# Optimization experiments

Hardware: AMD Instinct MI355X
Metric: run time of the kernel (lower is better)

## Reference

```python
import jax, jax.numpy as jnp
import numpy as np

HEAD_SIZE = 64
EMBED_DIM = 1024
SEQ_LEN = 4096
BATCH = 4


def setup_inputs() -> dict:
    key = jax.random.key(0)
    kx, kk, kq, kv = jax.random.split(key, 4)
    x = jax.random.normal(kx, (BATCH, SEQ_LEN, EMBED_DIM), dtype=jnp.float32)
    # nn.Linear(embedding_dim, head_size, bias=False): weight [head_size, embed];
    # store transposed [embed, head_size] so projection is x @ W.
    scale = 1.0 / np.sqrt(EMBED_DIM)
    Wk = jax.random.uniform(kk, (EMBED_DIM, HEAD_SIZE), jnp.float32, -scale, scale)
    Wq = jax.random.uniform(kq, (EMBED_DIM, HEAD_SIZE), jnp.float32, -scale, scale)
    Wv = jax.random.uniform(kv, (EMBED_DIM, HEAD_SIZE), jnp.float32, -scale, scale)
    return {"x": x, "Wk": Wk, "Wq": Wq, "Wv": Wv}


def reference(x, Wk, Wq, Wv):
    B, T, C = x.shape
    k = x @ Wk  # [B, T, H]
    q = x @ Wq  # [B, T, H]
    v = x @ Wv  # [B, T, H]
    H = k.shape[-1]
    s = jnp.einsum('bth,bsh->bts', q, k) * (H ** -0.5)  # [B, T, T]
    causal = jnp.tril(jnp.ones((T, T), dtype=bool))
    s = jnp.where(causal, s, -jnp.inf)
    a = jax.nn.softmax(s, axis=-1)  # dropout p=0.0 -> identity
    z = jnp.einsum('bts,bsh->bth', a, v)  # [B, T, H]
    return z
```

## Files before the change

### kernel.cpp

```cpp
#include <hip/hip_runtime.h>

#define SEQ 4096
#define EMB 1024
#define HS 64

typedef __attribute__((ext_vector_type(8))) short bf16x8;
typedef __attribute__((ext_vector_type(4))) float f32x4;

__device__ __forceinline__ unsigned short f2b(float f) {
    union { float f; unsigned u; } v; v.f = f;
    unsigned r = v.u + 0x7fffu + ((v.u >> 16) & 1u);
    return (unsigned short)(r >> 16);
}
__device__ __forceinline__ float b2f(unsigned short h) {
    union { unsigned u; float f; } v; v.u = ((unsigned)h) << 16;
    return v.f;
}
template <typename T>
__device__ __forceinline__ void gll16(const T* g, void* l) {
    __builtin_amdgcn_global_load_lds(
        (const __attribute__((address_space(1))) unsigned int*)(g),
        (__attribute__((address_space(3))) unsigned int*)(l), 16, 0, 0);
}

__global__ __launch_bounds__(256) void wt_kernel(const float* __restrict__ Wq,
                                                 const float* __restrict__ Wk,
                                                 const float* __restrict__ Wv,
                                                 unsigned short* __restrict__ Wt) {
    int id = blockIdx.x * 256 + threadIdx.x;
    int mat = id >> 16;
    int rem = id & 65535;
    int k = rem >> 6;
    int n = rem & 63;
    const float* W = (mat == 0) ? Wq : (mat == 1) ? Wk : Wv;
    float scale = (mat == 0) ? 0.125f * 1.44269504f : 1.0f;
    Wt[(mat * HS + n) * EMB + k] = f2b(W[k * HS + n] * scale);
}

__global__ __launch_bounds__(256, 2) void proj_kernel(const float* __restrict__ x,
                                                      const unsigned short* __restrict__ Wt,
                                                      unsigned short* __restrict__ Qb,
                                                      unsigned short* __restrict__ Kb,
                                                      unsigned short* __restrict__ Vt) {
    __shared__ float xf[2][32 * 64];
    __shared__ unsigned short wb[2][192 * 64];
    const int tid = threadIdx.x;
    const int wave = tid >> 6, lane = tid & 63;
    const int col = lane & 15, quad = lane >> 4;
    const int m0 = blockIdx.x * 32;
    const int b = m0 >> 12, t0 = m0 & 4095;

    const int xr_in = lane >> 4;
    const int xc = lane & 15;
    const int wr_in = lane >> 3;
    const int wc = lane & 7;

    f32x4 acc[2][3];
    #pragma unroll
    for (int i = 0; i < 2; i++)
        #pragma unroll
        for (int j = 0; j < 3; j++) acc[i][j] = (f32x4){0.f, 0.f, 0.f, 0.f};

    auto stage = [&](int k0, int bufi) {
        #pragma unroll
        for (int t = 0; t < 2; t++) {
            int R = (wave + t * 4) * 4;
            int row = R + xr_in;
            gll16(x + (size_t)(m0 + row) * EMB + k0 + ((xc ^ (row & 15)) << 2),
                  &xf[bufi][R * 64]);
        }
        #pragma unroll
        for (int t = 0; t < 6; t++) {
            int R = (wave * 6 + t) * 8;
            int row = R + wr_in;
            gll16(Wt + (size_t)row * EMB + k0 + ((wc ^ (row & 7)) << 3),
                  &wb[bufi][R * 64]);
        }
    };

    stage(0, 0);
    int buf = 0;
    #pragma unroll 1
    for (int k0 = 0; k0 < EMB; k0 += 64) {
        __syncthreads();
        if (k0 + 64 < EMB) stage(k0 + 64, buf ^ 1);
        #pragma unroll
        for (int kc = 0; kc < 2; kc++) {
            const int q2 = quad + kc * 4;
            bf16x8 af[2], bfr[3];
            #pragma unroll
            for (int mt = 0; mt < 2; mt++) {
                int rr = mt * 16 + col;
                float4 lo = *(const float4*)&xf[buf][rr * 64 + (((2 * q2) ^ col) << 2)];
                float4 hi = *(const float4*)&xf[buf][rr * 64 + (((2 * q2 + 1) ^ col) << 2)];
                bf16x8 a;
                a[0] = (short)f2b(lo.x); a[1] = (short)f2b(lo.y);
                a[2] = (short)f2b(lo.z); a[3] = (short)f2b(lo.w);
                a[4] = (short)f2b(hi.x); a[5] = (short)f2b(hi.y);
                a[6] = (short)f2b(hi.z); a[7] = (short)f2b(hi.w);
                af[mt] = a;
            }
            #pragma unroll
            for (int nt = 0; nt < 3; nt++) {
                int rn = wave * 48 + nt * 16 + col;
                bfr[nt] = *(const bf16x8*)&wb[buf][rn * 64 + ((q2 ^ (col & 7)) << 3)];
            }
            #pragma unroll
            for (int mt = 0; mt < 2; mt++)
                #pragma unroll
                for (int nt = 0; nt < 3; nt++)
                    acc[mt][nt] = __builtin_amdgcn_mfma_f32_16x16x32_bf16(af[mt], bfr[nt], acc[mt][nt], 0, 0, 0);
        }
        buf ^= 1;
    }

    #pragma unroll
    for (int mt = 0; mt < 2; mt++)
        #pragma unroll
        for (int nt = 0; nt < 3; nt++) {
            const int g = wave * 3 + nt;
            const int mat = g >> 2;
            const int ncol = (g & 3) * 16 + col;
            #pragma unroll
            for (int r = 0; r < 4; r++) {
                unsigned short val = f2b(acc[mt][nt][r]);
                int row = mt * 16 + quad * 4 + r;
                if (mat == 0)      Qb[(size_t)(m0 + row) * HS + ncol] = val;
                else if (mat == 1) Kb[(size_t)(m0 + row) * HS + ncol] = val;
                else               Vt[((size_t)b * HS + ncol) * SEQ + t0 + row] = val;
            }
        }
}

__global__ __launch_bounds__(256, 3) void attn_kernel(const unsigned short* __restrict__ Qb,
                                                      const unsigned short* __restrict__ Kb,
                                                      const unsigned short* __restrict__ Vt,
                                                      unsigned short* __restrict__ Opart,
                                                      float* __restrict__ Lpart) {
    __shared__ unsigned short Kl[2][64 * 64];
    __shared__ unsigned short Vl[2][64 * 64];
    __shared__ unsigned short P_lds[4][16 * 72];
    const int tid = threadIdx.x;
    const int wave = tid >> 6, lane = tid & 63;
    const int col = lane & 15, quad = lane >> 4;
    const int bid = blockIdx.x;
    const int g = 287 - (bid >> 2);
    const int b = bid & 3;
    int T = 0, accp = 0;
    for (;;) { int np = (T + 8) >> 3; if (accp + np > g) break; accp += np; T++; }
    const int piece = g - accp;
    const int q0 = T << 6;
    const int s_beg = piece << 3;
    const int s_end = min(s_beg + 8, T + 1);

    const unsigned short* Kp = Kb + ((size_t)(b << 12)) * HS;
    const unsigned short* Vp = Vt + (size_t)b * HS * SEQ;

    bf16x8 qf[2];
    #pragma unroll
    for (int c = 0; c < 2; c++)
        qf[c] = *(const bf16x8*)(Qb + ((size_t)(b << 12) + q0 + wave * 16 + col) * HS + quad * 8 + c * 32);

    f32x4 o[4];
    float l[4];
    #pragma unroll
    for (int ct = 0; ct < 4; ct++) o[ct] = (f32x4){0.f, 0.f, 0.f, 0.f};
    #pragma unroll
    for (int r = 0; r < 4; r++) l[r] = 0.f;

    const int r_in = lane >> 3;
    const int ch = lane & 7;

    auto stage = [&](int s, int bufi) {
        const int kv0 = s << 6;
        #pragma unroll
        for (int t = 0; t < 2; t++) {
            int R = (wave + t * 4) * 8;
            int row = R + r_in;
            gll16(Kp + (size_t)(kv0 + row) * HS + ((ch ^ (row & 7)) << 3), &Kl[bufi][R * 64]);
            gll16(Vp + (size_t)row * SEQ + kv0 + ((ch ^ (row & 7)) << 3), &Vl[bufi][R * 64]);
        }
    };

    stage(s_beg, 0);
    int buf = 0;
    const int rgb = q0 + wave * 16 + quad * 4;
    unsigned short* Pl = P_lds[wave];

    #pragma unroll 1
    for (int s = s_beg; s < s_end; s++) {
        __syncthreads();
        if (s + 1 < s_end) stage(s + 1, buf ^ 1);
        const int kv0 = s << 6;

        f32x4 sacc[4];
        #pragma unroll
        for (int ct = 0; ct < 4; ct++) sacc[ct] = (f32x4){0.f, 0.f, 0.f, 0.f};
        #pragma unroll
        for (int ct = 0; ct < 4; ct++) {
            int n = ct * 16 + col;
            #pragma unroll
            for (int kc = 0; kc < 2; kc++) {
                bf16x8 kf = *(const bf16x8*)&Kl[buf][n * 64 + (((kc * 4 + quad) ^ (col & 7)) << 3)];
                sacc[ct] = __builtin_amdgcn_mfma_f32_16x16x32_bf16(qf[kc], kf, sacc[ct], 0, 0, 0);
            }
        }

        float p[4][4];
        #pragma unroll
        for (int ct = 0; ct < 4; ct++) {
            int cg = kv0 + ct * 16 + col;
            #pragma unroll
            for (int r = 0; r < 4; r++) {
                float e = __builtin_exp2f(sacc[ct][r]);
                e = (cg > rgb + r) ? 0.f : e;
                p[ct][r] = e;
                l[r] += e;
            }
        }

        #pragma unroll
        for (int ct = 0; ct < 4; ct++)
            #pragma unroll
            for (int r = 0; r < 4; r++)
                Pl[(quad * 4 + r) * 72 + ct * 16 + col] = f2b(p[ct][r]);
        bf16x8 pf[2];
        #pragma unroll
        for (int c = 0; c < 2; c++)
            pf[c] = *(const bf16x8*)&Pl[col * 72 + quad * 8 + c * 32];

        #pragma unroll
        for (int ct = 0; ct < 4; ct++) {
            int h = ct * 16 + col;
            #pragma unroll
            for (int kc = 0; kc < 2; kc++) {
                bf16x8 vf = *(const bf16x8*)&Vl[buf][h * 64 + (((kc * 4 + quad) ^ (col & 7)) << 3)];
                o[ct] = __builtin_amdgcn_mfma_f32_16x16x32_bf16(pf[kc], vf, o[ct], 0, 0, 0);
            }
        }
        buf ^= 1;
    }

    #pragma unroll
    for (int off = 1; off < 16; off <<= 1)
        #pragma unroll
        for (int r = 0; r < 4; r++)
            l[r] += __shfl_xor(l[r], off, 64);

    unsigned short* Op = Opart + ((size_t)bid * 4 + wave) * 1024;
    #pragma unroll
    for (int ct = 0; ct < 4; ct++) {
        ushort4 st;
        st.x = f2b(o[ct][0]); st.y = f2b(o[ct][1]);
        st.z = f2b(o[ct][2]); st.w = f2b(o[ct][3]);
        *(ushort4*)(Op + ct * 256 + lane * 4) = st;
    }
    if (col == 0) {
        #pragma unroll
        for (int r = 0; r < 4; r++)
            Lpart[bid * 64 + wave * 16 + quad * 4 + r] = l[r];
    }
}

__global__ __launch_bounds__(256) void comb_kernel(const unsigned short* __restrict__ Opart,
                                                   const float* __restrict__ Lpart,
                                                   float* __restrict__ out) {
    int gid = blockIdx.x * 256 + threadIdx.x;
    int row = gid >> 4;
    int c4 = (gid & 15) * 4;
    int b = row >> 12;
    int t = row & 4095;
    int T = t >> 6;
    int rin = t & 63;
    int wv = rin >> 4;
    int r16 = rin & 15;
    int quad = r16 >> 2, rr = r16 & 3;
    int ct = c4 >> 4, col0 = c4 & 15;
    int qq = T >> 3, rm = T & 7;
    int base = T + ((qq * (qq - 1)) << 2) + rm * qq;
    int np = (T + 8) >> 3;

    float acc[4] = {0.f, 0.f, 0.f, 0.f};
    float l = 0.f;
    for (int p = 0; p < np; p++) {
        int gg = base + p;
        int idx = ((287 - gg) << 2) | b;
        const unsigned short* bs = Opart + ((size_t)idx * 4 + wv) * 1024 + ct * 256;
        #pragma unroll
        for (int j = 0; j < 4; j++)
            acc[j] += b2f(bs[(quad * 16 + col0 + j) * 4 + rr]);
        l += Lpart[idx * 64 + rin];
    }
    float inv = 1.f / l;
    float4 res = make_float4(acc[0] * inv, acc[1] * inv, acc[2] * inv, acc[3] * inv);
    *(float4*)(out + (size_t)row * HS + c4) = res;
}

extern "C" void kernel_launch(void* const* d_in, const int* in_sizes, int n_in,
                              void* d_out, int out_size, void* d_ws, size_t ws_size,
                              hipStream_t stream) {
    const float* x  = (const float*)d_in[0];
    const float* Wk = (const float*)d_in[1];
    const float* Wq = (const float*)d_in[2];
    const float* Wv = (const float*)d_in[3];
    float* out = (float*)d_out;

    char* ws = (char*)d_ws;
    unsigned short* Wt = (unsigned short*)(ws);
    unsigned short* Qb = (unsigned short*)(ws + 393216);
    unsigned short* Kb = (unsigned short*)(ws + 2490368);
    unsigned short* Vt = (unsigned short*)(ws + 4587520);
    unsigned short* Opart = (unsigned short*)(ws + 6684672);
    float* Lpart          = (float*)(ws + 16121856);

    wt_kernel<<<dim3(768), dim3(256), 0, stream>>>(Wq, Wk, Wv, Wt);
    proj_kernel<<<dim3(512), dim3(256), 0, stream>>>(x, Wt, Qb, Kb, Vt);
    attn_kernel<<<dim3(1152), dim3(256), 0, stream>>>(Qb, Kb, Vt, Opart, Lpart);
    comb_kernel<<<dim3(1024), dim3(256), 0, stream>>>(Opart, Lpart, out);
}
```

Before: 162.3 us.

## Double query tile to 128 rows per block with 8 waves sharing K/V tiles

The attention kernel now runs 512-thread blocks covering 128 query rows, so each staged 64-row K/V tile is shared by 8 waves instead of 4. This halves redundant K/V global loads and block count, and the split-K piece schedule is recomputed for the larger tiles. The combine kernel is rewritten to read partial outputs with vectorized ushort4 loads matching the per-wave layout. Risks are lower occupancy from bigger blocks, coarser load balance, and extra wasted work on diagonal tiles, since the causal boundary now spans a 128-row tile.

```diff
diff --git a/kernel.cpp b/kernel.cpp
--- a/kernel.cpp
+++ b/kernel.cpp
@@ -132,26 +132,26 @@
         }
 }
 
-__global__ __launch_bounds__(256, 3) void attn_kernel(const unsigned short* __restrict__ Qb,
+__global__ __launch_bounds__(512, 3) void attn_kernel(const unsigned short* __restrict__ Qb,
                                                       const unsigned short* __restrict__ Kb,
                                                       const unsigned short* __restrict__ Vt,
                                                       unsigned short* __restrict__ Opart,
                                                       float* __restrict__ Lpart) {
     __shared__ unsigned short Kl[2][64 * 64];
     __shared__ unsigned short Vl[2][64 * 64];
-    __shared__ unsigned short P_lds[4][16 * 72];
+    __shared__ unsigned short P_lds[8][16 * 72];
     const int tid = threadIdx.x;
     const int wave = tid >> 6, lane = tid & 63;
     const int col = lane & 15, quad = lane >> 4;
     const int bid = blockIdx.x;
-    const int g = 287 - (bid >> 2);
+    const int g = 143 - (bid >> 2);
     const int b = bid & 3;
     int T = 0, accp = 0;
-    for (;;) { int np = (T + 8) >> 3; if (accp + np > g) break; accp += np; T++; }
+    for (;;) { int np = (T >> 2) + 1; if (accp + np > g) break; accp += np; T++; }
     const int piece = g - accp;
-    const int q0 = T << 6;
+    const int q0 = T << 7;
     const int s_beg = piece << 3;
-    const int s_end = min(s_beg + 8, T + 1);
+    const int s_end = min(s_beg + 8, 2 * T + 2);
 
     const unsigned short* Kp = Kb + ((size_t)(b << 12)) * HS;
     const unsigned short* Vp = Vt + (size_t)b * HS * SEQ;
@@ -173,13 +173,10 @@
 
     auto stage = [&](int s, int bufi) {
         const int kv0 = s << 6;
-        #pragma unroll
-        for (int t = 0; t < 2; t++) {
-            int R = (wave + t * 4) * 8;
-            int row = R + r_in;
-            gll16(Kp + (size_t)(kv0 + row) * HS + ((ch ^ (row & 7)) << 3), &Kl[bufi][R * 64]);
-            gll16(Vp + (size_t)row * SEQ + kv0 + ((ch ^ (row & 7)) << 3), &Vl[bufi][R * 64]);
-        }
+        int R = wave * 8;
+        int row = R + r_in;
+        gll16(Kp + (size_t)(kv0 + row) * HS + ((ch ^ (row & 7)) << 3), &Kl[bufi][R * 64]);
+        gll16(Vp + (size_t)row * SEQ + kv0 + ((ch ^ (row & 7)) << 3), &Vl[bufi][R * 64]);
     };
 
     stage(s_beg, 0);
@@ -247,7 +244,8 @@
         for (int r = 0; r < 4; r++)
             l[r] += __shfl_xor(l[r], off, 64);
 
-    unsigned short* Op = Opart + ((size_t)bid * 4 + wave) * 1024;
+    const int widx = bid * 8 + wave;
+    unsigned short* Op = Opart + (size_t)widx * 1024;
     #pragma unroll
     for (int ct = 0; ct < 4; ct++) {
         ushort4 st;
@@ -258,42 +256,42 @@
     if (col == 0) {
         #pragma unroll
         for (int r = 0; r < 4; r++)
-            Lpart[bid * 64 + wave * 16 + quad * 4 + r] = l[r];
+            Lpart[widx * 16 + quad * 4 + r] = l[r];
     }
 }
 
 __global__ __launch_bounds__(256) void comb_kernel(const unsigned short* __restrict__ Opart,
                                                    const float* __restrict__ Lpart,
                                                    float* __restrict__ out) {
-    int gid = blockIdx.x * 256 + threadIdx.x;
-    int row = gid >> 4;
-    int c4 = (gid & 15) * 4;
-    int b = row >> 12;
-    int t = row & 4095;
-    int T = t >> 6;
-    int rin = t & 63;
-    int wv = rin >> 4;
-    int r16 = rin & 15;
-    int quad = r16 >> 2, rr = r16 & 3;
-    int ct = c4 >> 4, col0 = c4 & 15;
-    int qq = T >> 3, rm = T & 7;
-    int base = T + ((qq * (qq - 1)) << 2) + rm * qq;
-    int np = (T + 8) >> 3;
+    const int bid = blockIdx.x;
+    const int b = bid & 3;
+    const int T = (bid >> 2) & 31;
+    const int wave = bid >> 7;
+    const int tid = threadIdx.x;
+    const int lane = tid & 63, ct = tid >> 6;
+    const int col = lane & 15, quad = lane >> 4;
+
+    const int Q = T >> 2, R = T & 3;
+    const int base = T + 2 * Q * (Q - 1) + R * Q;
+    const int np = Q + 1;
 
     float acc[4] = {0.f, 0.f, 0.f, 0.f};
-    float l = 0.f;
+    float l[4] = {0.f, 0.f, 0.f, 0.f};
     for (int p = 0; p < np; p++) {
         int gg = base + p;
-        int idx = ((287 - gg) << 2) | b;
-        const unsigned short* bs = Opart + ((size_t)idx * 4 + wv) * 1024 + ct * 256;
-        #pragma unroll
-        for (int j = 0; j < 4; j++)
-            acc[j] += b2f(bs[(quad * 16 + col0 + j) * 4 + rr]);
-        l += Lpart[idx * 64 + rin];
-    }
-    float inv = 1.f / l;
-    float4 res = make_float4(acc[0] * inv, acc[1] * inv, acc[2] * inv, acc[3] * inv);
-    *(float4*)(out + (size_t)row * HS + c4) = res;
+        int bidp = ((143 - gg) << 2) | b;
+        int widx = bidp * 8 + wave;
+        ushort4 v = *(const ushort4*)(Opart + (size_t)widx * 1024 + ct * 256 + lane * 4);
+        acc[0] += b2f(v.x); acc[1] += b2f(v.y);
+        acc[2] += b2f(v.z); acc[3] += b2f(v.w);
+        #pragma unroll
+        for (int r = 0; r < 4; r++)
+            l[r] += Lpart[widx * 16 + quad * 4 + r];
+    }
+    const size_t rowb = (size_t)(b << 12) + (T << 7) + wave * 16 + quad * 4;
+    #pragma unroll
+    for (int r = 0; r < 4; r++)
+        out[(rowb + r) * HS + ct * 16 + col] = acc[r] / l[r];
 }
 
 extern "C" void kernel_launch(void* const* d_in, const int* in_sizes, int n_in,
@@ -315,6 +313,6 @@
 
     wt_kernel<<<dim3(768), dim3(256), 0, stream>>>(Wq, Wk, Wv, Wt);
     proj_kernel<<<dim3(512), dim3(256), 0, stream>>>(x, Wt, Qb, Kb, Vt);
-    attn_kernel<<<dim3(1152), dim3(256), 0, stream>>>(Qb, Kb, Vt, Opart, Lpart);
+    attn_kernel<<<dim3(576), dim3(512), 0, stream>>>(Qb, Kb, Vt, Opart, Lpart);
     comb_kernel<<<dim3(1024), dim3(256), 0, stream>>>(Opart, Lpart, out);
 }
```

Result: faster. 154.7 us (-4.7%).
